# Kernel optimization log

Hardware: AMD Instinct MI355X
Metric: run time of the kernel (lower is better)

## Reference

```python
import jax, jax.numpy as jnp
import numpy as np

B, T, D, H, L, FF, V = 32, 64, 512, 8, 4, 2048, 128
HD = D // H
TEMP = 0.1
SCALE_BASE = 16.0
NEG = -1e9


def setup_inputs() -> dict:
    key = jax.random.key(0)
    cnt = [0]
    def nk():
        cnt[0] += 1
        return jax.random.fold_in(key, cnt[0])
    def rn(shape, s=0.02):
        return jax.random.normal(nk(), shape, dtype=jnp.float32) * s
    inp = {
        "target_tensor": jax.random.randint(nk(), (B, T), 0, V),
        "mol_encoding": jax.random.normal(nk(), (B, D), dtype=jnp.float32),
        "emb": rn((V, D), 1.0),
        "sa_in_w": rn((L, 3 * D, D)), "sa_in_b": jnp.zeros((L, 3 * D), jnp.float32),
        "sa_out_w": rn((L, D, D)), "sa_out_b": jnp.zeros((L, D), jnp.float32),
        "ca_in_w": rn((L, 3 * D, D)), "ca_in_b": jnp.zeros((L, 3 * D), jnp.float32),
        "ca_out_w": rn((L, D, D)), "ca_out_b": jnp.zeros((L, D), jnp.float32),
        "ff_w1": rn((L, FF, D)), "ff_b1": jnp.zeros((L, FF), jnp.float32),
        "ff_w2": rn((L, D, FF)), "ff_b2": jnp.zeros((L, D), jnp.float32),
        "n1_g": jnp.ones((L, D), jnp.float32), "n1_b": jnp.zeros((L, D), jnp.float32),
        "n2_g": jnp.ones((L, D), jnp.float32), "n2_b": jnp.zeros((L, D), jnp.float32),
        "n3_g": jnp.ones((L, D), jnp.float32), "n3_b": jnp.zeros((L, D), jnp.float32),
        "fn_g": jnp.ones((D,), jnp.float32), "fn_b": jnp.zeros((D,), jnp.float32),
        "out_w1": rn((2 * D, D)), "out_b1": jnp.zeros((2 * D,), jnp.float32),
        "out_w2": rn((1024, 2 * D)), "out_b2": jnp.zeros((1024,), jnp.float32),
        "out_w3": rn((V, 1024)), "out_b3": jnp.zeros((V,), jnp.float32),
    }
    return inp


def _ln(x, g, b, eps=1e-5):
    mu = x.mean(-1, keepdims=True)
    var = ((x - mu) ** 2).mean(-1, keepdims=True)
    return (x - mu) * jax.lax.rsqrt(var + eps) * g + b


def _xpos(x):
    # x: [B, T, D]; XPOS rotary with scale_base=16, downscale=False
    t, d = x.shape[1], x.shape[2]
    half = d // 2
    sv = (jnp.arange(0, d, 2, dtype=jnp.float32) + 0.4 * d) / (1.4 * d)      # [half]
    pos = jnp.arange(t, dtype=jnp.float32)
    scale = sv[None, :] ** (pos / SCALE_BASE)[:, None]                       # [t, half]
    inv_freq = 1.0 / (10000.0 ** (jnp.arange(half, dtype=jnp.float32) / half))
    ang = pos[:, None] * inv_freq[None, :]                                   # [t, half]
    sin = jnp.repeat(jnp.sin(ang) * scale, 2, axis=-1)                       # duplicate_interleave
    cos = jnp.repeat(jnp.cos(ang) * scale, 2, axis=-1)
    x1, x2 = x[..., ::2], x[..., 1::2]
    rot = jnp.stack((-x2, x1), axis=-1).reshape(x.shape)                     # rotate_every_two
    return x * cos + rot * sin


def _mha(q_in, k_in, v_in, in_w, in_b, out_w, out_b, mask):
    wq, wk, wv = jnp.split(in_w, 3, axis=0)
    bq, bk, bv = jnp.split(in_b, 3, axis=0)
    Bq, Tq = q_in.shape[0], q_in.shape[1]
    q = (q_in @ wq.T + bq).reshape(Bq, Tq, H, HD)
    k = (k_in @ wk.T + bk).reshape(Bq, -1, H, HD)
    v = (v_in @ wv.T + bv).reshape(Bq, -1, H, HD)
    scores = jnp.einsum('bqhd,bkhd->bhqk', q, k) / np.float32(np.sqrt(HD))
    if mask is not None:
        scores = jnp.where(mask, NEG, scores)
    p = jax.nn.softmax(scores, axis=-1)
    o = jnp.einsum('bhqk,bkhd->bqhd', p, v).reshape(Bq, Tq, D)
    return o @ out_w.T + out_b


def reference(target_tensor, mol_encoding, emb, sa_in_w, sa_in_b, sa_out_w, sa_out_b,
              ca_in_w, ca_in_b, ca_out_w, ca_out_b, ff_w1, ff_b1, ff_w2, ff_b2,
              n1_g, n1_b, n2_g, n2_b, n3_g, n3_b, fn_g, fn_b,
              out_w1, out_b1, out_w2, out_b2, out_w3, out_b3):
    memory = mol_encoding[:, None, :]                      # [B, 1, D]
    causal = jnp.triu(jnp.ones((T, T), bool), 1)
    samp_key = jax.random.key(1)

    def logits_at(pred, t):
        x = _xpos(emb[pred])                               # [B, T, D]
        mask = causal[None, None] | (pred == 0)[:, None, None, :]
        for i in range(L):
            a = _mha(x, x, x, sa_in_w[i], sa_in_b[i], sa_out_w[i], sa_out_b[i], mask)
            x = _ln(x + a, n1_g[i], n1_b[i])
            c = _mha(x, memory, memory, ca_in_w[i], ca_in_b[i], ca_out_w[i], ca_out_b[i], None)
            x = _ln(x + c, n2_g[i], n2_b[i])
            f = jax.nn.silu(x @ ff_w1[i].T + ff_b1[i]) @ ff_w2[i].T + ff_b2[i]
            x = _ln(x + f, n3_g[i], n3_b[i])
        x = _ln(x, fn_g, fn_b)
        h = jnp.take(x, t - 1, axis=1)                     # [B, D]
        h = jax.nn.gelu(h @ out_w1.T + out_b1, approximate=False)
        h = jax.nn.gelu(h @ out_w2.T + out_b2, approximate=False)
        return h @ out_w3.T + out_b3                       # [B, V]

    def step(pred, t):
        logits = logits_at(pred, t)
        lp = jax.nn.log_softmax(logits / TEMP, axis=-1)
        u = jax.random.uniform(jax.random.fold_in(samp_key, t), lp.shape)
        g = -jnp.log(-jnp.log(u + 1e-9) + 1e-9)
        tok = jnp.argmax(lp + g, axis=-1).astype(jnp.int32)
        return pred.at[:, t].set(tok), logits

    pred0 = jnp.zeros((B, T), jnp.int32).at[:, 0].set(1)
    pred, _ = jax.lax.scan(jax.checkpoint(step), pred0, jnp.arange(1, T))
    return pred
```

## Files before the change

kernel.cpp:

```cpp
#include <hip/hip_runtime.h>
#include <stdint.h>
#include <stddef.h>

#define BB 32
#define TT 64
#define DD 512
#define HH 8
#define HDIM 64
#define LL 4
#define FFD 2048
#define VV 128

#define NBLK 256
#define NTHR 512

__host__ __device__ inline uint32_t rotl32(uint32_t v, int n){ return (v << n) | (v >> (32 - n)); }

__host__ __device__ inline void tf2x32(uint32_t k0, uint32_t k1, uint32_t x0, uint32_t x1,
                                       uint32_t* o0, uint32_t* o1){
  uint32_t ks2 = k0 ^ k1 ^ 0x1BD11BDAu;
  x0 += k0; x1 += k1;
  x0 += x1; x1 = rotl32(x1,13); x1 ^= x0;
  x0 += x1; x1 = rotl32(x1,15); x1 ^= x0;
  x0 += x1; x1 = rotl32(x1,26); x1 ^= x0;
// ... 23 lines not shown
}

__device__ inline float dot_f4(const float* __restrict__ a, const float* __restrict__ w, int K){
  float acc = 0.f;
  const float4* a4 = (const float4*)a;
  const float4* w4 = (const float4*)w;
  int K4 = K >> 2;
  for (int k = 0; k < K4; ++k){
    float4 av = a4[k], wv = w4[k];
    acc = fmaf(av.x, wv.x, acc);
    acc = fmaf(av.y, wv.y, acc);
    acc = fmaf(av.z, wv.z, acc);
    acc = fmaf(av.w, wv.w, acc);
  }
  return acc;
}

__device__ inline float block_ln(float v, float g, float bb, float* red){
  __syncthreads();
  float s = v;
  #pragma unroll
  for (int off = 32; off; off >>= 1) s += __shfl_xor(s, off);
  if ((threadIdx.x & 63) == 0) red[threadIdx.x >> 6] = s;
  __syncthreads();
  float mu = (red[0]+red[1]+red[2]+red[3]+red[4]+red[5]+red[6]+red[7]) * (1.0f/512.0f);
  float dv = v - mu;
  float sq = dv * dv;
  #pragma unroll
  for (int off = 32; off; off >>= 1) sq += __shfl_xor(sq, off);
  __syncthreads();
  if ((threadIdx.x & 63) == 0) red[threadIdx.x >> 6] = sq;
  __syncthreads();
  float var = (red[0]+red[1]+red[2]+red[3]+red[4]+red[5]+red[6]+red[7]) * (1.0f/512.0f);
  return dv * (1.0f / sqrtf(var + 1e-5f)) * g + bb;
}

__device__ inline float row_reduce(float v, int wid, int j, float* wred){
  #pragma unroll
  for (int off = 32; off; off >>= 1) v += __shfl_xor(v, off);
  if ((threadIdx.x & 63) == 0) wred[wid] = v;
  __syncthreads();
  float r = wred[2*j] + wred[2*j+1];
  __syncthreads();
  return r;
}

__device__ __forceinline__ void gbar(unsigned* bar, int g){
  __syncthreads();
  if (threadIdx.x == 0){
    unsigned* cnt = bar + g*64;
    unsigned* gen = bar + g*64 + 16;
    __builtin_amdgcn_fence(__ATOMIC_RELEASE, "agent");
    unsigned old = __hip_atomic_load(gen, __ATOMIC_RELAXED, __HIP_MEMORY_SCOPE_AGENT);
    if (__hip_atomic_fetch_add(cnt, 1u, __ATOMIC_RELAXED, __HIP_MEMORY_SCOPE_AGENT) == 31u){
      __hip_atomic_store(cnt, 0u, __ATOMIC_RELAXED, __HIP_MEMORY_SCOPE_AGENT);
      __hip_atomic_fetch_add(gen, 1u, __ATOMIC_RELEASE, __HIP_MEMORY_SCOPE_AGENT);
    } else {
      while (__hip_atomic_load(gen, __ATOMIC_RELAXED, __HIP_MEMORY_SCOPE_AGENT) == old)
        __builtin_amdgcn_s_sleep(1);
    }
    __builtin_amdgcn_fence(__ATOMIC_ACQUIRE, "agent");
  }
  __syncthreads();
}

__global__ void k_tables(float* __restrict__ cosb, float* __restrict__ sinb){
  int tid = blockIdx.x * blockDim.x + threadIdx.x;
  int p = tid >> 8, i = tid & 255;
  float sv = (2.0f * (float)i + 204.8f) / 716.8f;
  float scale = powf(sv, (float)p / 16.0f);
  float invf = 1.0f / powf(10000.0f, (float)i / 256.0f);
  float ang = (float)p * invf;
  cosb[tid] = cosf(ang) * scale;
  sinb[tid] = sinf(ang) * scale;
}

__global__ void k_ca1(const float* __restrict__ mol, const float* __restrict__ w,
                      const float* __restrict__ bias, float* __restrict__ tmp){
  int tid = blockIdx.x * blockDim.x + threadIdx.x;
  int l = tid >> 14; int r = tid & 16383; int b = r >> 9; int d = r & 511;
  const float* wr = w + (size_t)l*3*DD*DD + (size_t)(2*DD + d)*DD;
  tmp[tid] = bias[l*3*DD + 2*DD + d] + dot_f4(mol + (size_t)b*DD, wr, DD);
}

__global__ void k_ca2(const float* __restrict__ tmp, const float* __restrict__ w,
                      const float* __restrict__ bias, float* __restrict__ cac){
  int tid = blockIdx.x * blockDim.x + threadIdx.x;
  int l = tid >> 14; int r = tid & 16383; int b = r >> 9; int d = r & 511;
  const float* wr = w + (size_t)l*DD*DD + (size_t)d*DD;
  cac[tid] = bias[l*DD + d] + dot_f4(tmp + ((size_t)l*BB + b)*DD, wr, DD);
}

__global__ void k_binit(unsigned* __restrict__ bar, int* __restrict__ pred){
  int tid = threadIdx.x;
  bar[tid] = 0u;
  pred[tid]        = ((tid & (TT-1)) == 0) ? 1 : 0;
  pred[tid + 1024] = (((tid + 1024) & (TT-1)) == 0) ? 1 : 0;
}

__global__ void k_pack32(const float* __restrict__ in, float* __restrict__ out,
                         int N, int K, int total){
  int tid = blockIdx.x * blockDim.x + threadIdx.x;
  if (tid >= total) return;
  int S = N * K;
  int l = tid / S, r = tid - l*S;
  int k32 = r / (32*N);
  int r2 = r - k32*32*N;
  int n = r2 >> 5, ku = r2 & 31;
  out[tid] = in[(size_t)l*S + (size_t)n*K + k32*32 + ku];
}

#define CELL4(WARR, KOFF)                                                     \
  _Pragma("unroll")                                                           \
  for (int q = 0; q < 8; ++q){                                                \
    float4 w = WARR[q];                                                       \
    const int kk = (KOFF) + q*4;                                              \
    float4 xa = *(const float4*)&sxp[0*512 + kk];                             \
    float4 xb = *(const float4*)&sxp[1*512 + kk];                             \
    float4 xc = *(const float4*)&sxp[2*512 + kk];                             \
    float4 xd = *(const float4*)&sxp[3*512 + kk];                             \
    a0=fmaf(w.x,xa.x,a0); a0=fmaf(w.y,xa.y,a0); a0=fmaf(w.z,xa.z,a0); a0=fmaf(w.w,xa.w,a0); \
    a1=fmaf(w.x,xb.x,a1); a1=fmaf(w.y,xb.y,a1); a1=fmaf(w.z,xb.z,a1); a1=fmaf(w.w,xb.w,a1); \
    a2=fmaf(w.x,xc.x,a2); a2=fmaf(w.y,xc.y,a2); a2=fmaf(w.z,xc.z,a2); a2=fmaf(w.w,xc.w,a2); \
    a3=fmaf(w.x,xd.x,a3); a3=fmaf(w.y,xd.y,a3); a3=fmaf(w.z,xd.z,a3); a3=fmaf(w.w,xd.w,a3); \
  }

struct KParams {
  const float *emb, *sab, *sob, *f1b, *f2b;
  const float *g1,*b1,*g2,*b2,*g3,*b3,*fg,*fb;
  const float *o1b,*o2b,*o3w,*o3b;
  const float *cosb,*sinb,*cac;
  const float *sawP,*sowP,*f1wP,*f2wP,*o1wP,*o2wP;
  float *kc,*vc,*xl,*qb,*at,*ao,*x2,*fo,*h1,*xf,*hh1,*hh2,*ps3;
  int *pred;
  unsigned *bar;
};

__global__ __launch_bounds__(NTHR) void k_persist(KParams P){
  const int bid = blockIdx.x, tid = threadIdx.x;
  const int g = bid & 7;
  const int m = bid >> 3;
  const int wid = tid >> 6, lane = tid & 63;
  __shared__ __align__(16) float smem[8704];

  for (int t = 1; t < TT; ++t){
    const int pp = t - 1;

    for (int l = 0; l < LL; ++l){
      {
        float* sx   = smem;
        float* part = smem + 2048;
        float* srow = smem + 4096;
        const int j = tid >> 7, d4 = (tid & 127) * 4;
        const int rb = g*4 + j;
        if (l == 0){
          int tok = P.pred[rb*TT + pp];
          #pragma unroll
          for (int e = d4; e < d4 + 4; e += 2){
            int i = e >> 1;
            float c = P.cosb[pp*256 + i], s = P.sinb[pp*256 + i];
            float e0 = P.emb[(size_t)tok*DD + e];
            float e1 = P.emb[(size_t)tok*DD + e + 1];
            sx[j*512 + e]     = fmaf(e0, c, -(e1*s));
            sx[j*512 + e + 1] = fmaf(e1, c, e0*s);
          }
        } else {
          if (tid < 4){
            float a = 0.f, bq = 0.f;
            const float* pr = P.ps3 + (size_t)(g*4 + tid)*64;
            for (int s = 0; s < 32; ++s){ a += pr[s*2]; bq += pr[s*2+1]; }
            float mu = a * (1.0f/512.0f);
            float var = bq * (1.0f/512.0f) - mu*mu;
            srow[tid*2]   = mu;
            srow[tid*2+1] = 1.0f / sqrtf(var + 1e-5f);
          }
          __syncthreads();
          float mu = srow[j*2], rs = srow[j*2+1];
          float4 xv = *(const float4*)&P.x2[(size_t)rb*DD + d4];
          float4 fv = *(const float4*)&P.fo[(size_t)rb*DD + d4];
          const float* g3r = P.g3 + (size_t)(l-1)*DD;
          const float* b3r = P.b3 + (size_t)(l-1)*DD;
          float yv[4] = {xv.x+fv.x, xv.y+fv.y, xv.z+fv.z, xv.w+fv.w};
          #pragma unroll
          for (int i = 0; i < 4; ++i)
            sx[j*512 + d4 + i] = (yv[i]-mu)*rs*g3r[d4+i] + b3r[d4+i];
        }
        __syncthreads();
        if (m == 0){
          float4 v = *(float4*)&sx[j*512 + d4];
          *(float4*)&P.xl[(size_t)rb*DD + d4] = v;
        }
        if (m < 24){
          const int n0 = m*64;
          const float4* wb0 = (const float4*)P.sawP + ((size_t)l*16 + wid*2)*(1536*8)
                            + (size_t)(n0 + lane)*8;
          const float4* wb1 = wb0 + 1536*8;
          float4 w0[8], w1[8];
          #pragma unroll
          for (int q = 0; q < 8; ++q) w0[q] = wb0[q];
          #pragma unroll
          for (int q = 0; q < 8; ++q) w1[q] = wb1[q];
          float a0=0.f,a1=0.f,a2=0.f,a3=0.f;
          const float* sxp = sx;
          const int kb = wid*64;
          CELL4(w0, kb);
          CELL4(w1, kb + 32);
          part[(wid*4+0)*64 + lane] = a0;
          part[(wid*4+1)*64 + lane] = a1;
          part[(wid*4+2)*64 + lane] = a2;
          part[(wid*4+3)*64 + lane] = a3;
          __syncthreads();
          if (tid < 256){
            int jr = tid >> 6, nl = tid & 63;
            int n = n0 + nl, rb2 = g*4 + jr;
            float s = P.sab[l*1536 + n];
            #pragma unroll
            for (int w = 0; w < 8; ++w) s += part[(w*4+jr)*64 + nl];
            if (n < DD){
              P.qb[(size_t)rb2*DD + n] = s;
            } else if (n < 2*DD){
              int h = (n - DD) >> 6, hd = (n - DD) & 63;
              P.kc[((((size_t)l*BB + rb2)*HH + h)*TT + pp)*HDIM + hd] = s;
            } else {
              int h = (n - 2*DD) >> 6, hd = (n - 2*DD) & 63;
              P.vc[((((size_t)l*BB + rb2)*HH + h)*TT + pp)*HDIM + hd] = s;
            }
          }
        }
      }
      gbar(P.bar, g);

      {
        int bl = m >> 3, h = m & 7, rb = g*4 + bl;
        float* qs = smem; float* ps = smem + 64;
        if (tid < 64) qs[tid] = P.qb[(size_t)rb*DD + h*HDIM + tid];
        __syncthreads();
        if (tid < 64){
          const float* kb = P.kc + (((size_t)l*BB + rb)*HH + h)*TT*HDIM;
          float s = -INFINITY;
          if (lane <= pp && P.pred[rb*TT + lane] != 0){
            const float* kr = kb + lane*HDIM;
            float acc = 0.f;
            #pragma unroll
            for (int k2 = 0; k2 < HDIM; ++k2) acc = fmaf(qs[k2], kr[k2], acc);
            s = acc * 0.125f;
          }
          float mx = s;
          #pragma unroll
          for (int off = 32; off; off >>= 1) mx = fmaxf(mx, __shfl_xor(mx, off));
          float e = (s == -INFINITY) ? 0.f : expf(s - mx);
          float sum = e;
          #pragma unroll
          for (int off = 32; off; off >>= 1) sum += __shfl_xor(sum, off);
          ps[lane] = e / sum;
          const float* vb = P.vc + (((size_t)l*BB + rb)*HH + h)*TT*HDIM;
          float o = 0.f;
          int jj = 0;
          for (; jj + 8 <= t; jj += 8){
            float vv[8];
            #pragma unroll
            for (int u = 0; u < 8; ++u) vv[u] = vb[(jj+u)*HDIM + lane];
            #pragma unroll
            for (int u = 0; u < 8; ++u) o = fmaf(ps[jj+u], vv[u], o);
          }
          for (; jj <= pp; ++jj) o = fmaf(ps[jj], vb[jj*HDIM + lane], o);
          P.at[(size_t)rb*DD + h*HDIM + lane] = o;
        }
      }
      gbar(P.bar, g);

      {
        float* ats  = smem;
        float* part = smem + 2048;
        const int j = tid >> 7, d4 = (tid & 127) * 4;
        *(float4*)&ats[j*512 + d4] = *(const float4*)&P.at[(size_t)(g*4+j)*DD + d4];
        __syncthreads();
        const int n0 = m*16;
        const int jb = lane >> 4, nc = lane & 15;
        const float4* wb0 = (const float4*)P.sowP + ((size_t)l*16 + wid*2)*(512*8)
                          + (size_t)(n0 + nc)*8;
        const float4* wb1 = wb0 + 512*8;
        float4 w0[8], w1[8];
        #pragma unroll
        for (int q = 0; q < 8; ++q) w0[q] = wb0[q];
        #pragma unroll
        for (int q = 0; q < 8; ++q) w1[q] = wb1[q];
        float acc = 0.f;
        const int kb = wid*64;
        #pragma unroll
        for (int q = 0; q < 8; ++q){
          float4 w = w0[q];
          float4 xa = *(const float4*)&ats[jb*512 + kb + q*4];
          acc=fmaf(w.x,xa.x,acc); acc=fmaf(w.y,xa.y,acc); acc=fmaf(w.z,xa.z,acc); acc=fmaf(w.w,xa.w,acc);
        }
        #pragma unroll
        for (int q = 0; q < 8; ++q){
          float4 w = w1[q];
          float4 xa = *(const float4*)&ats[jb*512 + kb + 32 + q*4];
          acc=fmaf(w.x,xa.x,acc); acc=fmaf(w.y,xa.y,acc); acc=fmaf(w.z,xa.z,acc); acc=fmaf(w.w,xa.w,acc);
        }
        part[wid*64 + lane] = acc;
        __syncthreads();
        if (tid < 64){
          int jb2 = tid >> 4, nc2 = tid & 15, n = n0 + nc2;
          float s = P.sob[l*DD + n];
          #pragma unroll
          for (int w = 0; w < 8; ++w) s += part[w*64 + jb2*16 + nc2];
          P.ao[(size_t)(g*4+jb2)*DD + n] = s;
        }
      }
      gbar(P.bar, g);

      {
        float* sx2  = smem;
        float* part = smem + 2048;
        float* wred = smem + 4096;
        const int j = tid >> 7, d4 = (tid & 127) * 4;
        const int rb = g*4 + j;
        float4 xlv = *(const float4*)&P.xl[(size_t)rb*DD + d4];
        float4 aov = *(const float4*)&P.ao[(size_t)rb*DD + d4];
        float y[4] = {xlv.x+aov.x, xlv.y+aov.y, xlv.z+aov.z, xlv.w+aov.w};
        float s = ((y[0]+y[1])+y[2])+y[3];
        float mu = row_reduce(s, wid, j, wred) * (1.0f/512.0f);
        float dv[4], sq = 0.f;
        #pragma unroll
        for (int i = 0; i < 4; ++i){ dv[i] = y[i]-mu; sq += dv[i]*dv[i]; }
        float rs = 1.0f / sqrtf(row_reduce(sq, wid, j, wred) * (1.0f/512.0f) + 1e-5f);
        float z[4];
        #pragma unroll
        for (int i = 0; i < 4; ++i){
          int d = d4 + i;
          z[i] = dv[i]*rs*P.g1[l*DD+d] + P.b1[l*DD+d] + P.cac[((size_t)l*BB + rb)*DD + d];
        }
        float s2 = ((z[0]+z[1])+z[2])+z[3];
        float mu2 = row_reduce(s2, wid, j, wred) * (1.0f/512.0f);
        float dz[4], sq2 = 0.f;
        #pragma unroll
        for (int i = 0; i < 4; ++i){ dz[i] = z[i]-mu2; sq2 += dz[i]*dz[i]; }
        float rs2 = 1.0f / sqrtf(row_reduce(sq2, wid, j, wred) * (1.0f/512.0f) + 1e-5f);
        float x2v[4];
        #pragma unroll
        for (int i = 0; i < 4; ++i){
          int d = d4 + i;
          x2v[i] = dz[i]*rs2*P.g2[l*DD+d] + P.b2[l*DD+d];
          sx2[j*512 + d] = x2v[i];
        }
        if (m == 0) *(float4*)&P.x2[(size_t)rb*DD + d4] = make_float4(x2v[0],x2v[1],x2v[2],x2v[3]);
        __syncthreads();
        const int n0 = m*64;
        const float4* wb0 = (const float4*)P.f1wP + ((size_t)l*16 + wid*2)*(2048*8)
                          + (size_t)(n0 + lane)*8;
        const float4* wb1 = wb0 + 2048*8;
        float4 w0[8], w1[8];
        #pragma unroll
        for (int q = 0; q < 8; ++q) w0[q] = wb0[q];
        #pragma unroll
        for (int q = 0; q < 8; ++q) w1[q] = wb1[q];
        float a0=0.f,a1=0.f,a2=0.f,a3=0.f;
        const float* sxp = sx2;
        const int kb = wid*64;
        CELL4(w0, kb);
        CELL4(w1, kb + 32);
        part[(wid*4+0)*64 + lane] = a0;
        part[(wid*4+1)*64 + lane] = a1;
        part[(wid*4+2)*64 + lane] = a2;
        part[(wid*4+3)*64 + lane] = a3;
        __syncthreads();
        if (tid < 256){
          int jr = tid >> 6, nl = tid & 63;
          int n = n0 + nl;
          float v = P.f1b[l*FFD + n];
          #pragma unroll
          for (int w = 0; w < 8; ++w) v += part[(w*4+jr)*64 + nl];
          P.h1[(size_t)(g*4+jr)*FFD + n] = v / (1.0f + expf(-v));
        }
      }
      gbar(P.bar, g);

      {
        float* sh1  = smem;
        float* part = smem + 8192;
        #pragma unroll
        for (int q = 0; q < 4; ++q){
          int fi = tid + q*512;
          int j = fi >> 9, c4 = fi & 511;
          *(float4*)&sh1[j*2048 + c4*4] = *(const float4*)&P.h1[(size_t)(g*4+j)*FFD + c4*4];
        }
        __syncthreads();
        const int n0 = m*16;
        const int jb = lane >> 4, nc = lane & 15;
        const float4* base = (const float4*)P.f2wP + ((size_t)l*64 + wid*8)*(512*8)
                           + (size_t)(n0 + nc)*8;
        float acc = 0.f;
        #pragma unroll
        for (int cc = 0; cc < 4; ++cc){
          const float4* b0 = base + (size_t)(cc*2)*(512*8);
          const float4* b1 = b0 + 512*8;
          float4 w0[8], w1[8];
          #pragma unroll
          for (int q = 0; q < 8; ++q) w0[q] = b0[q];
          #pragma unroll
          for (int q = 0; q < 8; ++q) w1[q] = b1[q];
          const int kb = wid*256 + cc*64;
          #pragma unroll
          for (int q = 0; q < 8; ++q){
            float4 w = w0[q];
            float4 xa = *(const float4*)&sh1[jb*2048 + kb + q*4];
            acc=fmaf(w.x,xa.x,acc); acc=fmaf(w.y,xa.y,acc); acc=fmaf(w.z,xa.z,acc); acc=fmaf(w.w,xa.w,acc);
          }
          #pragma unroll
          for (int q = 0; q < 8; ++q){
            float4 w = w1[q];
            float4 xa = *(const float4*)&sh1[jb*2048 + kb + 32 + q*4];
            acc=fmaf(w.x,xa.x,acc); acc=fmaf(w.y,xa.y,acc); acc=fmaf(w.z,xa.z,acc); acc=fmaf(w.w,xa.w,acc);
          }
        }
        part[wid*64 + lane] = acc;
        __syncthreads();
        if (tid < 64){
          int jb2 = tid >> 4, nc2 = tid & 15, n = n0 + nc2;
          int rb2 = g*4 + jb2;
          float val = P.f2b[l*DD + n];
          #pragma unroll
          for (int w = 0; w < 8; ++w) val += part[w*64 + jb2*16 + nc2];
          P.fo[(size_t)rb2*DD + n] = val;
          float y = P.x2[(size_t)rb2*DD + n] + val;
          float s1 = y, sq = y*y;
          #pragma unroll
          for (int off = 1; off < 16; off <<= 1){
            s1 += __shfl_xor(s1, off);
            sq += __shfl_xor(sq, off);
          }
          if (nc2 == 0){
            P.ps3[(size_t)(rb2*32 + m)*2]     = s1;
            P.ps3[(size_t)(rb2*32 + m)*2 + 1] = sq;
          }
        }
      }
      gbar(P.bar, g);
    }

    if (m < 4){
      int rb = g*4 + m, d = tid;
      float y = P.x2[(size_t)rb*DD + d] + P.fo[(size_t)rb*DD + d];
      float xv = block_ln(y, P.g3[3*DD + d], P.b3[3*DD + d], smem);
      float o  = block_ln(xv, P.fg[d], P.fb[d], smem);
      P.xf[(size_t)rb*DD + d] = o;
    }
    gbar(P.bar, g);

    {
      float* sxf  = smem;
      float* part = smem + 2048;
      const int j = tid >> 7, d4 = (tid & 127) * 4;
      *(float4*)&sxf[j*512 + d4] = *(const float4*)&P.xf[(size_t)(g*4+j)*DD + d4];
      __syncthreads();
      const int n0 = m*32;
      const int jh = lane >> 5, nc = lane & 31;
      const float4* wb0 = (const float4*)P.o1wP + (size_t)(wid*2)*(1024*8)
                        + (size_t)(n0 + nc)*8;
      const float4* wb1 = wb0 + 1024*8;
      float4 w0[8], w1[8];
      #pragma unroll
      for (int q = 0; q < 8; ++q) w0[q] = wb0[q];
      #pragma unroll
      for (int q = 0; q < 8; ++q) w1[q] = wb1[q];
      float ac0 = 0.f, ac1 = 0.f;
      const int kb = wid*64;
      #pragma unroll
      for (int q = 0; q < 8; ++q){
        float4 w = w0[q];
        float4 xa = *(const float4*)&sxf[jh*512 + kb + q*4];
        float4 xb = *(const float4*)&sxf[(jh+2)*512 + kb + q*4];
        ac0=fmaf(w.x,xa.x,ac0); ac0=fmaf(w.y,xa.y,ac0); ac0=fmaf(w.z,xa.z,ac0); ac0=fmaf(w.w,xa.w,ac0);
        ac1=fmaf(w.x,xb.x,ac1); ac1=fmaf(w.y,xb.y,ac1); ac1=fmaf(w.z,xb.z,ac1); ac1=fmaf(w.w,xb.w,ac1);
      }
      #pragma unroll
      for (int q = 0; q < 8; ++q){
        float4 w = w1[q];
        float4 xa = *(const float4*)&sxf[jh*512 + kb + 32 + q*4];
        float4 xb = *(const float4*)&sxf[(jh+2)*512 + kb + 32 + q*4];
        ac0=fmaf(w.x,xa.x,ac0); ac0=fmaf(w.y,xa.y,ac0); ac0=fmaf(w.z,xa.z,ac0); ac0=fmaf(w.w,xa.w,ac0);
        ac1=fmaf(w.x,xb.x,ac1); ac1=fmaf(w.y,xb.y,ac1); ac1=fmaf(w.z,xb.z,ac1); ac1=fmaf(w.w,xb.w,ac1);
      }
      part[(wid*2+0)*64 + lane] = ac0;
      part[(wid*2+1)*64 + lane] = ac1;
      __syncthreads();
      if (tid < 128){
        int row = tid >> 5, nc2 = tid & 31;
        int r = row >> 1, jh2 = row & 1;
        float s = P.o1b[n0 + nc2];
        #pragma unroll
        for (int w = 0; w < 8; ++w) s += part[(w*2+r)*64 + jh2*32 + nc2];
        float a = s;
        P.hh1[(size_t)(g*4+row)*1024 + n0 + nc2] = 0.5f * a * (1.0f + erff(a / 1.41421356237309504880f));
      }
    }
    gbar(P.bar, g);

    {
      float* sh   = smem;
      float* part = smem + 4096;
      #pragma unroll
      for (int q = 0; q < 2; ++q){
        int fi = tid + q*512;
        int j = fi >> 8, c4 = fi & 255;
        *(float4*)&sh[j*1024 + c4*4] = *(const float4*)&P.hh1[(size_t)(g*4+j)*1024 + c4*4];
      }
      __syncthreads();
      const int n0 = m*32;
      const int jh = lane >> 5, nc = lane & 31;
      const float4* base = (const float4*)P.o2wP + (size_t)(wid*4)*(1024*8)
                         + (size_t)(n0 + nc)*8;
      float ac0 = 0.f, ac1 = 0.f;
      #pragma unroll
      for (int cc = 0; cc < 2; ++cc){
        const float4* b0 = base + (size_t)(cc*2)*(1024*8);
        const float4* b1 = b0 + 1024*8;
        float4 w0[8], w1[8];
        #pragma unroll
        for (int q = 0; q < 8; ++q) w0[q] = b0[q];
        #pragma unroll
        for (int q = 0; q < 8; ++q) w1[q] = b1[q];
        const int kb = wid*128 + cc*64;
        #pragma unroll
        for (int q = 0; q < 8; ++q){
          float4 w = w0[q];
          float4 xa = *(const float4*)&sh[jh*1024 + kb + q*4];
          float4 xb = *(const float4*)&sh[(jh+2)*1024 + kb + q*4];
          ac0=fmaf(w.x,xa.x,ac0); ac0=fmaf(w.y,xa.y,ac0); ac0=fmaf(w.z,xa.z,ac0); ac0=fmaf(w.w,xa.w,ac0);
          ac1=fmaf(w.x,xb.x,ac1); ac1=fmaf(w.y,xb.y,ac1); ac1=fmaf(w.z,xb.z,ac1); ac1=fmaf(w.w,xb.w,ac1);
        }
        #pragma unroll
        for (int q = 0; q < 8; ++q){
          float4 w = w1[q];
          float4 xa = *(const float4*)&sh[jh*1024 + kb + 32 + q*4];
          float4 xb = *(const float4*)&sh[(jh+2)*1024 + kb + 32 + q*4];
          ac0=fmaf(w.x,xa.x,ac0); ac0=fmaf(w.y,xa.y,ac0); ac0=fmaf(w.z,xa.z,ac0); ac0=fmaf(w.w,xa.w,ac0);
          ac1=fmaf(w.x,xb.x,ac1); ac1=fmaf(w.y,xb.y,ac1); ac1=fmaf(w.z,xb.z,ac1); ac1=fmaf(w.w,xb.w,ac1);
        }
      }
      part[(wid*2+0)*64 + lane] = ac0;
      part[(wid*2+1)*64 + lane] = ac1;
      __syncthreads();
      if (tid < 128){
        int row = tid >> 5, nc2 = tid & 31;
        int r = row >> 1, jh2 = row & 1;
        float s = P.o2b[n0 + nc2];
        #pragma unroll
        for (int w = 0; w < 8; ++w) s += part[(w*2+r)*64 + jh2*32 + nc2];
        float a = s;
        P.hh2[(size_t)(g*4+row)*1024 + n0 + nc2] = 0.5f * a * (1.0f + erff(a / 1.41421356237309504880f));
      }
    }
    gbar(P.bar, g);

    if (m < 4){
      int rb = g*4 + m, v = tid;
      float* hrow = smem;
      float* red  = smem + 1024;
      int*   redi = (int*)(smem + 1032);
      for (int k = tid; k < 1024; k += NTHR) hrow[k] = P.hh2[(size_t)rb*1024 + k];
      __syncthreads();
      float sv = 0.f;
      if (tid < 128){
        float acc = P.o3b[v] + dot_f4(hrow, P.o3w + (size_t)v*1024, 1024);
        sv = acc / 0.1f;
      }
      float mx = (tid < 128) ? sv : -INFINITY;
      #pragma unroll
      for (int off = 32; off; off >>= 1) mx = fmaxf(mx, __shfl_xor(mx, off));
      __syncthreads();
      if (tid < 128 && (tid & 63) == 0) red[tid >> 6] = mx;
      __syncthreads();
      mx = fmaxf(red[0], red[1]);
      float e = (tid < 128) ? expf(sv - mx) : 0.f;
      float sum = e;
      #pragma unroll
      for (int off = 32; off; off >>= 1) sum += __shfl_xor(sum, off);
      __syncthreads();
      if (tid < 128 && (tid & 63) == 0) red[tid >> 6] = sum;
      __syncthreads();
      sum = red[0] + red[1];
      float bv = -INFINITY; int bi = 0x7fffffff;
      if (tid < 128){
        float lp = (sv - mx) - logf(sum);
        uint32_t kk0, kk1, o0, o1;
        tf2x32(0u, 1u, 0u, (uint32_t)t, &kk0, &kk1);
        tf2x32(kk0, kk1, 0u, (uint32_t)(rb*VV + v), &o0, &o1);
        uint32_t bits = o0 ^ o1;
        float u = __uint_as_float((bits >> 9) | 0x3F800000u) - 1.0f;
        float gg = -logf(-logf(u + 1e-9f) + 1e-9f);
        bv = lp + gg; bi = v;
      }
      #pragma unroll
      for (int off = 32; off; off >>= 1){
        float ov = __shfl_xor(bv, off);
        int   oi = __shfl_xor(bi, off);
        if (ov > bv || (ov == bv && oi < bi)){ bv = ov; bi = oi; }
      }
      __syncthreads();
      if (tid < 128 && (tid & 63) == 0){ red[tid >> 6] = bv; redi[tid >> 6] = bi; }
      __syncthreads();
      if (tid == 0){
        float v0 = red[0], v1 = red[1]; int i0 = redi[0], i1 = redi[1];
        P.pred[rb*TT + t] = (v1 > v0 || (v1 == v0 && i1 < i0)) ? i1 : i0;
      }
    }
    gbar(P.bar, g);
  }
}
// ... 88 lines not shown
```

Measured before the change: 23.45 ms.

## Regroup persistent blocks into 4 groups of 8 batch rows each

Changes the persistent kernel's partition from 8 groups of 4 batch rows to 4 groups of 8 rows, with 64 blocks per group sharing a group barrier. Each block now applies its register-held weight tile to 8 rows instead of 4, which halves the total weight traffic per step. In exchange each group barrier has more participants, many blocks sit idle in phases that cover only 24 or 32 column tiles, and shared memory use roughly doubles.

```diff
diff --git a/kernel.cpp b/kernel.cpp
--- a/kernel.cpp
+++ b/kernel.cpp
@@ -99,7 +99,7 @@
     unsigned* gen = bar + g*64 + 16;
     __builtin_amdgcn_fence(__ATOMIC_RELEASE, "agent");
     unsigned old = __hip_atomic_load(gen, __ATOMIC_RELAXED, __HIP_MEMORY_SCOPE_AGENT);
-    if (__hip_atomic_fetch_add(cnt, 1u, __ATOMIC_RELAXED, __HIP_MEMORY_SCOPE_AGENT) == 31u){
+    if (__hip_atomic_fetch_add(cnt, 1u, __ATOMIC_RELAXED, __HIP_MEMORY_SCOPE_AGENT) == 63u){
       __hip_atomic_store(cnt, 0u, __ATOMIC_RELAXED, __HIP_MEMORY_SCOPE_AGENT);
       __hip_atomic_fetch_add(gen, 1u, __ATOMIC_RELEASE, __HIP_MEMORY_SCOPE_AGENT);
     } else {
@@ -157,19 +157,17 @@
   out[tid] = in[(size_t)l*S + (size_t)n*K + k32*32 + ku];
 }
 
-#define CELL4(WARR, KOFF)                                                     \
+#define CELL8(WARR, KOFF)                                                     \
   _Pragma("unroll")                                                           \
   for (int q = 0; q < 8; ++q){                                                \
     float4 w = WARR[q];                                                       \
     const int kk = (KOFF) + q*4;                                              \
-    float4 xa = *(const float4*)&sxp[0*512 + kk];                             \
-    float4 xb = *(const float4*)&sxp[1*512 + kk];                             \
-    float4 xc = *(const float4*)&sxp[2*512 + kk];                             \
-    float4 xd = *(const float4*)&sxp[3*512 + kk];                             \
-    a0=fmaf(w.x,xa.x,a0); a0=fmaf(w.y,xa.y,a0); a0=fmaf(w.z,xa.z,a0); a0=fmaf(w.w,xa.w,a0); \
-    a1=fmaf(w.x,xb.x,a1); a1=fmaf(w.y,xb.y,a1); a1=fmaf(w.z,xb.z,a1); a1=fmaf(w.w,xb.w,a1); \
-    a2=fmaf(w.x,xc.x,a2); a2=fmaf(w.y,xc.y,a2); a2=fmaf(w.z,xc.z,a2); a2=fmaf(w.w,xc.w,a2); \
-    a3=fmaf(w.x,xd.x,a3); a3=fmaf(w.y,xd.y,a3); a3=fmaf(w.z,xd.z,a3); a3=fmaf(w.w,xd.w,a3); \
+    _Pragma("unroll")                                                         \
+    for (int r_ = 0; r_ < 8; ++r_){                                           \
+      float4 x = *(const float4*)&sxp[r_*512 + kk];                           \
+      a[r_]=fmaf(w.x,x.x,a[r_]); a[r_]=fmaf(w.y,x.y,a[r_]);                   \
+      a[r_]=fmaf(w.z,x.z,a[r_]); a[r_]=fmaf(w.w,x.w,a[r_]);                   \
+    }                                                                         \
   }
 
 struct KParams {
@@ -185,100 +183,107 @@
 
 __global__ __launch_bounds__(NTHR) void k_persist(KParams P){
   const int bid = blockIdx.x, tid = threadIdx.x;
-  const int g = bid & 7;
-  const int m = bid >> 3;
+  const int g = bid & 3;
+  const int m = bid >> 2;
   const int wid = tid >> 6, lane = tid & 63;
-  __shared__ __align__(16) float smem[8704];
+  __shared__ __align__(16) float smem[17472];
 
   for (int t = 1; t < TT; ++t){
     const int pp = t - 1;
 
     for (int l = 0; l < LL; ++l){
-      {
+      if (m < 24){
         float* sx   = smem;
-        float* part = smem + 2048;
-        float* srow = smem + 4096;
-        const int j = tid >> 7, d4 = (tid & 127) * 4;
-        const int rb = g*4 + j;
+        float* part = smem + 4096;
+        float* srow = smem + 8192;
         if (l == 0){
-          int tok = P.pred[rb*TT + pp];
-          #pragma unroll
-          for (int e = d4; e < d4 + 4; e += 2){
-            int i = e >> 1;
-            float c = P.cosb[pp*256 + i], s = P.sinb[pp*256 + i];
-            float e0 = P.emb[(size_t)tok*DD + e];
-            float e1 = P.emb[(size_t)tok*DD + e + 1];
-            sx[j*512 + e]     = fmaf(e0, c, -(e1*s));
-            sx[j*512 + e + 1] = fmaf(e1, c, e0*s);
+          #pragma unroll
+          for (int it = 0; it < 2; ++it){
+            int j = it*4 + (tid >> 7), d4 = (tid & 127) * 4;
+            int rb = g*8 + j;
+            int tok = P.pred[rb*TT + pp];
+            #pragma unroll
+            for (int e = d4; e < d4 + 4; e += 2){
+              int i = e >> 1;
+              float c = P.cosb[pp*256 + i], s = P.sinb[pp*256 + i];
+              float e0 = P.emb[(size_t)tok*DD + e];
+              float e1 = P.emb[(size_t)tok*DD + e + 1];
+              sx[j*512 + e]     = fmaf(e0, c, -(e1*s));
+              sx[j*512 + e + 1] = fmaf(e1, c, e0*s);
+            }
           }
         } else {
-          if (tid < 4){
-            float a = 0.f, bq = 0.f;
-            const float* pr = P.ps3 + (size_t)(g*4 + tid)*64;
-            for (int s = 0; s < 32; ++s){ a += pr[s*2]; bq += pr[s*2+1]; }
-            float mu = a * (1.0f/512.0f);
+          if (tid < 8){
+            float aa = 0.f, bq = 0.f;
+            const float* pr = P.ps3 + (size_t)(g*8 + tid)*64;
+            for (int s = 0; s < 32; ++s){ aa += pr[s*2]; bq += pr[s*2+1]; }
+            float mu = aa * (1.0f/512.0f);
             float var = bq * (1.0f/512.0f) - mu*mu;
             srow[tid*2]   = mu;
             srow[tid*2+1] = 1.0f / sqrtf(var + 1e-5f);
           }
           __syncthreads();
-          float mu = srow[j*2], rs = srow[j*2+1];
-          float4 xv = *(const float4*)&P.x2[(size_t)rb*DD + d4];
-          float4 fv = *(const float4*)&P.fo[(size_t)rb*DD + d4];
-          const float* g3r = P.g3 + (size_t)(l-1)*DD;
-          const float* b3r = P.b3 + (size_t)(l-1)*DD;
-          float yv[4] = {xv.x+fv.x, xv.y+fv.y, xv.z+fv.z, xv.w+fv.w};
-          #pragma unroll
-          for (int i = 0; i < 4; ++i)
-            sx[j*512 + d4 + i] = (yv[i]-mu)*rs*g3r[d4+i] + b3r[d4+i];
+          #pragma unroll
+          for (int it = 0; it < 2; ++it){
+            int j = it*4 + (tid >> 7), d4 = (tid & 127) * 4;
+            int rb = g*8 + j;
+            float mu = srow[j*2], rs = srow[j*2+1];
+            float4 xv = *(const float4*)&P.x2[(size_t)rb*DD + d4];
+            float4 fv = *(const float4*)&P.fo[(size_t)rb*DD + d4];
+            const float* g3r = P.g3 + (size_t)(l-1)*DD;
+            const float* b3r = P.b3 + (size_t)(l-1)*DD;
+            float yv[4] = {xv.x+fv.x, xv.y+fv.y, xv.z+fv.z, xv.w+fv.w};
+            #pragma unroll
+            for (int i = 0; i < 4; ++i)
+              sx[j*512 + d4 + i] = (yv[i]-mu)*rs*g3r[d4+i] + b3r[d4+i];
+          }
         }
         __syncthreads();
         if (m == 0){
-          float4 v = *(float4*)&sx[j*512 + d4];
-          *(float4*)&P.xl[(size_t)rb*DD + d4] = v;
-        }
-        if (m < 24){
-          const int n0 = m*64;
-          const float4* wb0 = (const float4*)P.sawP + ((size_t)l*16 + wid*2)*(1536*8)
-                            + (size_t)(n0 + lane)*8;
-          const float4* wb1 = wb0 + 1536*8;
-          float4 w0[8], w1[8];
-          #pragma unroll
-          for (int q = 0; q < 8; ++q) w0[q] = wb0[q];
-          #pragma unroll
-          for (int q = 0; q < 8; ++q) w1[q] = wb1[q];
-          float a0=0.f,a1=0.f,a2=0.f,a3=0.f;
-          const float* sxp = sx;
-          const int kb = wid*64;
-          CELL4(w0, kb);
-          CELL4(w1, kb + 32);
-          part[(wid*4+0)*64 + lane] = a0;
-          part[(wid*4+1)*64 + lane] = a1;
-          part[(wid*4+2)*64 + lane] = a2;
-          part[(wid*4+3)*64 + lane] = a3;
-          __syncthreads();
-          if (tid < 256){
-            int jr = tid >> 6, nl = tid & 63;
-            int n = n0 + nl, rb2 = g*4 + jr;
-            float s = P.sab[l*1536 + n];
-            #pragma unroll
-            for (int w = 0; w < 8; ++w) s += part[(w*4+jr)*64 + nl];
-            if (n < DD){
-              P.qb[(size_t)rb2*DD + n] = s;
-            } else if (n < 2*DD){
-              int h = (n - DD) >> 6, hd = (n - DD) & 63;
-              P.kc[((((size_t)l*BB + rb2)*HH + h)*TT + pp)*HDIM + hd] = s;
-            } else {
-              int h = (n - 2*DD) >> 6, hd = (n - 2*DD) & 63;
-              P.vc[((((size_t)l*BB + rb2)*HH + h)*TT + pp)*HDIM + hd] = s;
-            }
+          #pragma unroll
+          for (int it = 0; it < 2; ++it){
+            int j = it*4 + (tid >> 7), d4 = (tid & 127) * 4;
+            *(float4*)&P.xl[(size_t)(g*8+j)*DD + d4] = *(float4*)&sx[j*512 + d4];
+          }
+        }
+        const int n0 = m*64;
+        const float4* wb0 = (const float4*)P.sawP + ((size_t)l*16 + wid*2)*(1536*8)
+                          + (size_t)(n0 + lane)*8;
+        const float4* wb1 = wb0 + 1536*8;
+        float4 w0[8], w1[8];
+        #pragma unroll
+        for (int q = 0; q < 8; ++q) w0[q] = wb0[q];
+        #pragma unroll
+        for (int q = 0; q < 8; ++q) w1[q] = wb1[q];
+        float a[8] = {0.f,0.f,0.f,0.f,0.f,0.f,0.f,0.f};
+        const float* sxp = sx;
+        const int kb = wid*64;
+        CELL8(w0, kb);
+        CELL8(w1, kb + 32);
+        #pragma unroll
+        for (int r_ = 0; r_ < 8; ++r_) part[(wid*8 + r_)*64 + lane] = a[r_];
+        __syncthreads();
+        {
+          int jr = tid >> 6, nl = tid & 63;
+          int n = n0 + nl, rb2 = g*8 + jr;
+          float s = P.sab[l*1536 + n];
+          #pragma unroll
+          for (int w = 0; w < 8; ++w) s += part[(w*8+jr)*64 + nl];
+          if (n < DD){
+            P.qb[(size_t)rb2*DD + n] = s;
+          } else if (n < 2*DD){
+            int h = (n - DD) >> 6, hd = (n - DD) & 63;
+            P.kc[((((size_t)l*BB + rb2)*HH + h)*TT + pp)*HDIM + hd] = s;
+          } else {
+            int h = (n - 2*DD) >> 6, hd = (n - 2*DD) & 63;
+            P.vc[((((size_t)l*BB + rb2)*HH + h)*TT + pp)*HDIM + hd] = s;
           }
         }
       }
       gbar(P.bar, g);
 
       {
-        int bl = m >> 3, h = m & 7, rb = g*4 + bl;
+        int bl = m >> 3, h = m & 7, rb = g*8 + bl;
         float* qs = smem; float* ps = smem + 64;
         if (tid < 64) qs[tid] = P.qb[(size_t)rb*DD + h*HDIM + tid];
         __syncthreads();
@@ -316,11 +321,15 @@
       }
       gbar(P.bar, g);
 
-      {
+      if (m < 32){
         float* ats  = smem;
-        float* part = smem + 2048;
-        const int j = tid >> 7, d4 = (tid & 127) * 4;
-        *(float4*)&ats[j*512 + d4] = *(const float4*)&P.at[(size_t)(g*4+j)*DD + d4];
+        float* part = smem + 4096;
+        #pragma unroll
+        for (int q = 0; q < 2; ++q){
+          int fi = tid + q*512;
+          int j = fi >> 7, c4 = fi & 127;
+          *(float4*)&ats[j*512 + c4*4] = *(const float4*)&P.at[(size_t)(g*8+j)*DD + c4*4];
+        }
         __syncthreads();
         const int n0 = m*16;
         const int jb = lane >> 4, nc = lane & 15;
@@ -332,68 +341,82 @@
         for (int q = 0; q < 8; ++q) w0[q] = wb0[q];
         #pragma unroll
         for (int q = 0; q < 8; ++q) w1[q] = wb1[q];
-        float acc = 0.f;
+        float ac0 = 0.f, ac1 = 0.f;
         const int kb = wid*64;
         #pragma unroll
         for (int q = 0; q < 8; ++q){
           float4 w = w0[q];
           float4 xa = *(const float4*)&ats[jb*512 + kb + q*4];
-          acc=fmaf(w.x,xa.x,acc); acc=fmaf(w.y,xa.y,acc); acc=fmaf(w.z,xa.z,acc); acc=fmaf(w.w,xa.w,acc);
+          float4 xb = *(const float4*)&ats[(jb+4)*512 + kb + q*4];
+          ac0=fmaf(w.x,xa.x,ac0); ac0=fmaf(w.y,xa.y,ac0); ac0=fmaf(w.z,xa.z,ac0); ac0=fmaf(w.w,xa.w,ac0);
+          ac1=fmaf(w.x,xb.x,ac1); ac1=fmaf(w.y,xb.y,ac1); ac1=fmaf(w.z,xb.z,ac1); ac1=fmaf(w.w,xb.w,ac1);
         }
         #pragma unroll
         for (int q = 0; q < 8; ++q){
           float4 w = w1[q];
           float4 xa = *(const float4*)&ats[jb*512 + kb + 32 + q*4];
-          acc=fmaf(w.x,xa.x,acc); acc=fmaf(w.y,xa.y,acc); acc=fmaf(w.z,xa.z,acc); acc=fmaf(w.w,xa.w,acc);
-        }
-        part[wid*64 + lane] = acc;
-        __syncthreads();
-        if (tid < 64){
+          float4 xb = *(const float4*)&ats[(jb+4)*512 + kb + 32 + q*4];
+          ac0=fmaf(w.x,xa.x,ac0); ac0=fmaf(w.y,xa.y,ac0); ac0=fmaf(w.z,xa.z,ac0); ac0=fmaf(w.w,xa.w,ac0);
+          ac1=fmaf(w.x,xb.x,ac1); ac1=fmaf(w.y,xb.y,ac1); ac1=fmaf(w.z,xb.z,ac1); ac1=fmaf(w.w,xb.w,ac1);
+        }
+        part[wid*128 + jb*16 + nc]       = ac0;
+        part[wid*128 + (jb+4)*16 + nc]   = ac1;
+        __syncthreads();
+        if (tid < 128){
           int jb2 = tid >> 4, nc2 = tid & 15, n = n0 + nc2;
           float s = P.sob[l*DD + n];
           #pragma unroll
-          for (int w = 0; w < 8; ++w) s += part[w*64 + jb2*16 + nc2];
-          P.ao[(size_t)(g*4+jb2)*DD + n] = s;
+          for (int w = 0; w < 8; ++w) s += part[w*128 + jb2*16 + nc2];
+          P.ao[(size_t)(g*8+jb2)*DD + n] = s;
         }
       }
       gbar(P.bar, g);
 
-      {
+      if (m < 32){
         float* sx2  = smem;
-        float* part = smem + 2048;
-        float* wred = smem + 4096;
-        const int j = tid >> 7, d4 = (tid & 127) * 4;
-        const int rb = g*4 + j;
-        float4 xlv = *(const float4*)&P.xl[(size_t)rb*DD + d4];
-        float4 aov = *(const float4*)&P.ao[(size_t)rb*DD + d4];
-        float y[4] = {xlv.x+aov.x, xlv.y+aov.y, xlv.z+aov.z, xlv.w+aov.w};
-        float s = ((y[0]+y[1])+y[2])+y[3];
-        float mu = row_reduce(s, wid, j, wred) * (1.0f/512.0f);
-        float dv[4], sq = 0.f;
-        #pragma unroll
-        for (int i = 0; i < 4; ++i){ dv[i] = y[i]-mu; sq += dv[i]*dv[i]; }
-        float rs = 1.0f / sqrtf(row_reduce(sq, wid, j, wred) * (1.0f/512.0f) + 1e-5f);
-        float z[4];
-        #pragma unroll
-        for (int i = 0; i < 4; ++i){
-          int d = d4 + i;
-          z[i] = dv[i]*rs*P.g1[l*DD+d] + P.b1[l*DD+d] + P.cac[((size_t)l*BB + rb)*DD + d];
-        }
-        float s2 = ((z[0]+z[1])+z[2])+z[3];
-        float mu2 = row_reduce(s2, wid, j, wred) * (1.0f/512.0f);
-        float dz[4], sq2 = 0.f;
-        #pragma unroll
-        for (int i = 0; i < 4; ++i){ dz[i] = z[i]-mu2; sq2 += dz[i]*dz[i]; }
-        float rs2 = 1.0f / sqrtf(row_reduce(sq2, wid, j, wred) * (1.0f/512.0f) + 1e-5f);
-        float x2v[4];
-        #pragma unroll
-        for (int i = 0; i < 4; ++i){
-          int d = d4 + i;
-          x2v[i] = dz[i]*rs2*P.g2[l*DD+d] + P.b2[l*DD+d];
-          sx2[j*512 + d] = x2v[i];
-        }
-        if (m == 0) *(float4*)&P.x2[(size_t)rb*DD + d4] = make_float4(x2v[0],x2v[1],x2v[2],x2v[3]);
-        __syncthreads();
+        float* part = smem + 4096;
+        float* wred = smem + 8192;
+        #pragma unroll
+        for (int it = 0; it < 2; ++it){
+          int j = tid >> 7, d4 = (tid & 127) * 4;
+          int jr = it*4 + j;
+          int rb = g*8 + jr;
+          float4 xlv = *(const float4*)&P.xl[(size_t)rb*DD + d4];
+          float4 aov = *(const float4*)&P.ao[(size_t)rb*DD + d4];
+          float y[4] = {xlv.x+aov.x, xlv.y+aov.y, xlv.z+aov.z, xlv.w+aov.w};
+          float s = ((y[0]+y[1])+y[2])+y[3];
+          float mu = row_reduce(s, wid, j, wred) * (1.0f/512.0f);
+          float dv[4], sq = 0.f;
+          #pragma unroll
+          for (int i = 0; i < 4; ++i){ dv[i] = y[i]-mu; sq += dv[i]*dv[i]; }
+          float rs = 1.0f / sqrtf(row_reduce(sq, wid, j, wred) * (1.0f/512.0f) + 1e-5f);
+          float z[4];
+          #pragma unroll
+          for (int i = 0; i < 4; ++i){
+            int d = d4 + i;
+            z[i] = dv[i]*rs*P.g1[l*DD+d] + P.b1[l*DD+d] + P.cac[((size_t)l*BB + rb)*DD + d];
+          }
+          float s2 = ((z[0]+z[1])+z[2])+z[3];
+          float mu2 = row_reduce(s2, wid, j, wred) * (1.0f/512.0f);
+          float dz[4], sq2 = 0.f;
+          #pragma unroll
+          for (int i = 0; i < 4; ++i){ dz[i] = z[i]-mu2; sq2 += dz[i]*dz[i]; }
+          float rs2 = 1.0f / sqrtf(row_reduce(sq2, wid, j, wred) * (1.0f/512.0f) + 1e-5f);
+          #pragma unroll
+          for (int i = 0; i < 4; ++i){
+            int d = d4 + i;
+            float x2v = dz[i]*rs2*P.g2[l*DD+d] + P.b2[l*DD+d];
+            sx2[jr*512 + d] = x2v;
+          }
+        }
+        __syncthreads();
+        if (m == 0){
+          #pragma unroll
+          for (int it = 0; it < 2; ++it){
+            int jr = it*4 + (tid >> 7), d4 = (tid & 127) * 4;
+            *(float4*)&P.x2[(size_t)(g*8+jr)*DD + d4] = *(float4*)&sx2[jr*512 + d4];
+          }
+        }
         const int n0 = m*64;
         const float4* wb0 = (const float4*)P.f1wP + ((size_t)l*16 + wid*2)*(2048*8)
                           + (size_t)(n0 + lane)*8;
@@ -403,42 +426,40 @@
         for (int q = 0; q < 8; ++q) w0[q] = wb0[q];
         #pragma unroll
         for (int q = 0; q < 8; ++q) w1[q] = wb1[q];
-        float a0=0.f,a1=0.f,a2=0.f,a3=0.f;
+        float a[8] = {0.f,0.f,0.f,0.f,0.f,0.f,0.f,0.f};
         const float* sxp = sx2;
         const int kb = wid*64;
-        CELL4(w0, kb);
-        CELL4(w1, kb + 32);
-        part[(wid*4+0)*64 + lane] = a0;
-        part[(wid*4+1)*64 + lane] = a1;
-        part[(wid*4+2)*64 + lane] = a2;
-        part[(wid*4+3)*64 + lane] = a3;
-        __syncthreads();
-        if (tid < 256){
+        CELL8(w0, kb);
+        CELL8(w1, kb + 32);
+        #pragma unroll
+        for (int r_ = 0; r_ < 8; ++r_) part[(wid*8 + r_)*64 + lane] = a[r_];
+        __syncthreads();
+        {
           int jr = tid >> 6, nl = tid & 63;
           int n = n0 + nl;
           float v = P.f1b[l*FFD + n];
           #pragma unroll
-          for (int w = 0; w < 8; ++w) v += part[(w*4+jr)*64 + nl];
-          P.h1[(size_t)(g*4+jr)*FFD + n] = v / (1.0f + expf(-v));
+          for (int w = 0; w < 8; ++w) v += part[(w*8+jr)*64 + nl];
+          P.h1[(size_t)(g*8+jr)*FFD + n] = v / (1.0f + expf(-v));
         }
       }
       gbar(P.bar, g);
 
-      {
+      if (m < 32){
         float* sh1  = smem;
-        float* part = smem + 8192;
-        #pragma unroll
-        for (int q = 0; q < 4; ++q){
+        float* part = smem + 16384;
+        #pragma unroll
+        for (int q = 0; q < 8; ++q){
           int fi = tid + q*512;
           int j = fi >> 9, c4 = fi & 511;
-          *(float4*)&sh1[j*2048 + c4*4] = *(const float4*)&P.h1[(size_t)(g*4+j)*FFD + c4*4];
+          *(float4*)&sh1[j*2048 + c4*4] = *(const float4*)&P.h1[(size_t)(g*8+j)*FFD + c4*4];
         }
         __syncthreads();
         const int n0 = m*16;
         const int jb = lane >> 4, nc = lane & 15;
         const float4* base = (const float4*)P.f2wP + ((size_t)l*64 + wid*8)*(512*8)
                            + (size_t)(n0 + nc)*8;
-        float acc = 0.f;
+        float ac0 = 0.f, ac1 = 0.f;
         #pragma unroll
         for (int cc = 0; cc < 4; ++cc){
           const float4* b0 = base + (size_t)(cc*2)*(512*8);
@@ -453,23 +474,28 @@
           for (int q = 0; q < 8; ++q){
             float4 w = w0[q];
             float4 xa = *(const float4*)&sh1[jb*2048 + kb + q*4];
-            acc=fmaf(w.x,xa.x,acc); acc=fmaf(w.y,xa.y,acc); acc=fmaf(w.z,xa.z,acc); acc=fmaf(w.w,xa.w,acc);
+            float4 xb = *(const float4*)&sh1[(jb+4)*2048 + kb + q*4];
+            ac0=fmaf(w.x,xa.x,ac0); ac0=fmaf(w.y,xa.y,ac0); ac0=fmaf(w.z,xa.z,ac0); ac0=fmaf(w.w,xa.w,ac0);
+            ac1=fmaf(w.x,xb.x,ac1); ac1=fmaf(w.y,xb.y,ac1); ac1=fmaf(w.z,xb.z,ac1); ac1=fmaf(w.w,xb.w,ac1);
           }
           #pragma unroll
           for (int q = 0; q < 8; ++q){
             float4 w = w1[q];
             float4 xa = *(const float4*)&sh1[jb*2048 + kb + 32 + q*4];
-            acc=fmaf(w.x,xa.x,acc); acc=fmaf(w.y,xa.y,acc); acc=fmaf(w.z,xa.z,acc); acc=fmaf(w.w,xa.w,acc);
-          }
-        }
-        part[wid*64 + lane] = acc;
-        __syncthreads();
-        if (tid < 64){
+            float4 xb = *(const float4*)&sh1[(jb+4)*2048 + kb + 32 + q*4];
+            ac0=fmaf(w.x,xa.x,ac0); ac0=fmaf(w.y,xa.y,ac0); ac0=fmaf(w.z,xa.z,ac0); ac0=fmaf(w.w,xa.w,ac0);
+            ac1=fmaf(w.x,xb.x,ac1); ac1=fmaf(w.y,xb.y,ac1); ac1=fmaf(w.z,xb.z,ac1); ac1=fmaf(w.w,xb.w,ac1);
+          }
+        }
+        part[wid*128 + jb*16 + nc]     = ac0;
+        part[wid*128 + (jb+4)*16 + nc] = ac1;
+        __syncthreads();
+        if (tid < 128){
           int jb2 = tid >> 4, nc2 = tid & 15, n = n0 + nc2;
-          int rb2 = g*4 + jb2;
+          int rb2 = g*8 + jb2;
           float val = P.f2b[l*DD + n];
           #pragma unroll
-          for (int w = 0; w < 8; ++w) val += part[w*64 + jb2*16 + nc2];
+          for (int w = 0; w < 8; ++w) val += part[w*128 + jb2*16 + nc2];
           P.fo[(size_t)rb2*DD + n] = val;
           float y = P.x2[(size_t)rb2*DD + n] + val;
           float s1 = y, sq = y*y;
@@ -487,8 +513,8 @@
       gbar(P.bar, g);
     }
 
-    if (m < 4){
-      int rb = g*4 + m, d = tid;
+    if (m < 8){
+      int rb = g*8 + m, d = tid;
       float y = P.x2[(size_t)rb*DD + d] + P.fo[(size_t)rb*DD + d];
       float xv = block_ln(y, P.g3[3*DD + d], P.b3[3*DD + d], smem);
       float o  = block_ln(xv, P.fg[d], P.fb[d], smem);
@@ -496,11 +522,15 @@
     }
     gbar(P.bar, g);
 
-    {
+    if (m < 32){
       float* sxf  = smem;
-      float* part = smem + 2048;
-      const int j = tid >> 7, d4 = (tid & 127) * 4;
-      *(float4*)&sxf[j*512 + d4] = *(const float4*)&P.xf[(size_t)(g*4+j)*DD + d4];
+      float* part = smem + 4096;
+      #pragma unroll
+      for (int q = 0; q < 2; ++q){
+        int fi = tid + q*512;
+        int j = fi >> 7, c4 = fi & 127;
+        *(float4*)&sxf[j*512 + c4*4] = *(const float4*)&P.xf[(size_t)(g*8+j)*DD + c4*4];
+      }
       __syncthreads();
       const int n0 = m*32;
       const int jh = lane >> 5, nc = lane & 31;
@@ -512,54 +542,56 @@
       for (int q = 0; q < 8; ++q) w0[q] = wb0[q];
       #pragma unroll
       for (int q = 0; q < 8; ++q) w1[q] = wb1[q];
-      float ac0 = 0.f, ac1 = 0.f;
+      float ac[4] = {0.f,0.f,0.f,0.f};
       const int kb = wid*64;
       #pragma unroll
       for (int q = 0; q < 8; ++q){
         float4 w = w0[q];
-        float4 xa = *(const float4*)&sxf[jh*512 + kb + q*4];
-        float4 xb = *(const float4*)&sxf[(jh+2)*512 + kb + q*4];
-        ac0=fmaf(w.x,xa.x,ac0); ac0=fmaf(w.y,xa.y,ac0); ac0=fmaf(w.z,xa.z,ac0); ac0=fmaf(w.w,xa.w,ac0);
-        ac1=fmaf(w.x,xb.x,ac1); ac1=fmaf(w.y,xb.y,ac1); ac1=fmaf(w.z,xb.z,ac1); ac1=fmaf(w.w,xb.w,ac1);
+        #pragma unroll
+        for (int ai = 0; ai < 4; ++ai){
+          float4 x = *(const float4*)&sxf[(jh+2*ai)*512 + kb + q*4];
+          ac[ai]=fmaf(w.x,x.x,ac[ai]); ac[ai]=fmaf(w.y,x.y,ac[ai]);
+          ac[ai]=fmaf(w.z,x.z,ac[ai]); ac[ai]=fmaf(w.w,x.w,ac[ai]);
+        }
       }
       #pragma unroll
       for (int q = 0; q < 8; ++q){
         float4 w = w1[q];
-        float4 xa = *(const float4*)&sxf[jh*512 + kb + 32 + q*4];
-        float4 xb = *(const float4*)&sxf[(jh+2)*512 + kb + 32 + q*4];
-        ac0=fmaf(w.x,xa.x,ac0); ac0=fmaf(w.y,xa.y,ac0); ac0=fmaf(w.z,xa.z,ac0); ac0=fmaf(w.w,xa.w,ac0);
-        ac1=fmaf(w.x,xb.x,ac1); ac1=fmaf(w.y,xb.y,ac1); ac1=fmaf(w.z,xb.z,ac1); ac1=fmaf(w.w,xb.w,ac1);
-      }
-      part[(wid*2+0)*64 + lane] = ac0;
-      part[(wid*2+1)*64 + lane] = ac1;
-      __syncthreads();
-      if (tid < 128){
-        int row = tid >> 5, nc2 = tid & 31;
-        int r = row >> 1, jh2 = row & 1;
-        float s = P.o1b[n0 + nc2];
-        #pragma unroll
-        for (int w = 0; w < 8; ++w) s += part[(w*2+r)*64 + jh2*32 + nc2];
-        float a = s;
-        P.hh1[(size_t)(g*4+row)*1024 + n0 + nc2] = 0.5f * a * (1.0f + erff(a / 1.41421356237309504880f));
+        #pragma unroll
+        for (int ai = 0; ai < 4; ++ai){
+          float4 x = *(const float4*)&sxf[(jh+2*ai)*512 + kb + 32 + q*4];
+          ac[ai]=fmaf(w.x,x.x,ac[ai]); ac[ai]=fmaf(w.y,x.y,ac[ai]);
+          ac[ai]=fmaf(w.z,x.z,ac[ai]); ac[ai]=fmaf(w.w,x.w,ac[ai]);
+        }
+      }
+      #pragma unroll
+      for (int ai = 0; ai < 4; ++ai) part[(wid*8 + (jh+2*ai))*32 + nc] = ac[ai];
+      __syncthreads();
+      if (tid < 256){
+        int row = tid >> 5, nc2 = tid & 31, n = n0 + nc2;
+        float aa = P.o1b[n];
+        #pragma unroll
+        for (int w = 0; w < 8; ++w) aa += part[(w*8+row)*32 + nc2];
+        P.hh1[(size_t)(g*8+row)*1024 + n] = 0.5f * aa * (1.0f + erff(aa / 1.41421356237309504880f));
       }
     }
     gbar(P.bar, g);
 
-    {
+    if (m < 32){
       float* sh   = smem;
-      float* part = smem + 4096;
-      #pragma unroll
-      for (int q = 0; q < 2; ++q){
+      float* part = smem + 8192;
+      #pragma unroll
+      for (int q = 0; q < 4; ++q){
         int fi = tid + q*512;
         int j = fi >> 8, c4 = fi & 255;
-        *(float4*)&sh[j*1024 + c4*4] = *(const float4*)&P.hh1[(size_t)(g*4+j)*1024 + c4*4];
+        *(float4*)&sh[j*1024 + c4*4] = *(const float4*)&P.hh1[(size_t)(g*8+j)*1024 + c4*4];
       }
       __syncthreads();
       const int n0 = m*32;
       const int jh = lane >> 5, nc = lane & 31;
       const float4* base = (const float4*)P.o2wP + (size_t)(wid*4)*(1024*8)
                          + (size_t)(n0 + nc)*8;
-      float ac0 = 0.f, ac1 = 0.f;
+      float ac[4] = {0.f,0.f,0.f,0.f};
       #pragma unroll
       for (int cc = 0; cc < 2; ++cc){
         const float4* b0 = base + (size_t)(cc*2)*(1024*8);
@@ -573,37 +605,39 @@
         #pragma unroll
         for (int q = 0; q < 8; ++q){
           float4 w = w0[q];
-          float4 xa = *(const float4*)&sh[jh*1024 + kb + q*4];
-          float4 xb = *(const float4*)&sh[(jh+2)*1024 + kb + q*4];
-          ac0=fmaf(w.x,xa.x,ac0); ac0=fmaf(w.y,xa.y,ac0); ac0=fmaf(w.z,xa.z,ac0); ac0=fmaf(w.w,xa.w,ac0);
-          ac1=fmaf(w.x,xb.x,ac1); ac1=fmaf(w.y,xb.y,ac1); ac1=fmaf(w.z,xb.z,ac1); ac1=fmaf(w.w,xb.w,ac1);
+          #pragma unroll
+          for (int ai = 0; ai < 4; ++ai){
+            float4 x = *(const float4*)&sh[(jh+2*ai)*1024 + kb + q*4];
+            ac[ai]=fmaf(w.x,x.x,ac[ai]); ac[ai]=fmaf(w.y,x.y,ac[ai]);
+            ac[ai]=fmaf(w.z,x.z,ac[ai]); ac[ai]=fmaf(w.w,x.w,ac[ai]);
+          }
         }
         #pragma unroll
         for (int q = 0; q < 8; ++q){
           float4 w = w1[q];
-          float4 xa = *(const float4*)&sh[jh*1024 + kb + 32 + q*4];
-          float4 xb = *(const float4*)&sh[(jh+2)*1024 + kb + 32 + q*4];
-          ac0=fmaf(w.x,xa.x,ac0); ac0=fmaf(w.y,xa.y,ac0); ac0=fmaf(w.z,xa.z,ac0); ac0=fmaf(w.w,xa.w,ac0);
-          ac1=fmaf(w.x,xb.x,ac1); ac1=fmaf(w.y,xb.y,ac1); ac1=fmaf(w.z,xb.z,ac1); ac1=fmaf(w.w,xb.w,ac1);
-        }
-      }
-      part[(wid*2+0)*64 + lane] = ac0;
-      part[(wid*2+1)*64 + lane] = ac1;
-      __syncthreads();
-      if (tid < 128){
-        int row = tid >> 5, nc2 = tid & 31;
-        int r = row >> 1, jh2 = row & 1;
-        float s = P.o2b[n0 + nc2];
-        #pragma unroll
-        for (int w = 0; w < 8; ++w) s += part[(w*2+r)*64 + jh2*32 + nc2];
-        float a = s;
-        P.hh2[(size_t)(g*4+row)*1024 + n0 + nc2] = 0.5f * a * (1.0f + erff(a / 1.41421356237309504880f));
+          #pragma unroll
+          for (int ai = 0; ai < 4; ++ai){
+            float4 x = *(const float4*)&sh[(jh+2*ai)*1024 + kb + 32 + q*4];
+            ac[ai]=fmaf(w.x,x.x,ac[ai]); ac[ai]=fmaf(w.y,x.y,ac[ai]);
+            ac[ai]=fmaf(w.z,x.z,ac[ai]); ac[ai]=fmaf(w.w,x.w,ac[ai]);
+          }
+        }
+      }
+      #pragma unroll
+      for (int ai = 0; ai < 4; ++ai) part[(wid*8 + (jh+2*ai))*32 + nc] = ac[ai];
+      __syncthreads();
+      if (tid < 256){
+        int row = tid >> 5, nc2 = tid & 31, n = n0 + nc2;
+        float aa = P.o2b[n];
+        #pragma unroll
+        for (int w = 0; w < 8; ++w) aa += part[(w*8+row)*32 + nc2];
+        P.hh2[(size_t)(g*8+row)*1024 + n] = 0.5f * aa * (1.0f + erff(aa / 1.41421356237309504880f));
       }
     }
     gbar(P.bar, g);
 
-    if (m < 4){
-      int rb = g*4 + m, v = tid;
+    if (m < 8){
+      int rb = g*8 + m, v = tid;
       float* hrow = smem;
       float* red  = smem + 1024;
       int*   redi = (int*)(smem + 1032);
```

After: 26.35 ms. 1.12x slower.
